# Kernel tuning notes

Measured on AMD Instinct MI355X. Metric: run time of the kernel, lower is better.

## Reference

```python
import jax, jax.numpy as jnp
import numpy as np

B, L, D, N = 8, 1024, 1024, 32  # N = d_state // 2 (complex conjugate-pair modes)
DT_MIN, DT_MAX = 0.001, 0.1


def setup_inputs() -> dict:
    key = jax.random.key(0)
    ks = jax.random.split(key, 12)
    s = 1.0 / np.sqrt(D)  # torch Linear / Conv1d default init bound
    inp = {
        "x": jax.random.normal(ks[0], (B, L, D), jnp.float32),
        "in_W": jax.random.uniform(ks[1], (D, D), jnp.float32, -s, s),
        "in_b": jax.random.uniform(ks[2], (D,), jnp.float32, -s, s),
        # S4D kernel params
        "log_dt": (np.log(DT_MIN)
                   + jax.random.uniform(ks[3], (D,), jnp.float32)
                   * (np.log(DT_MAX) - np.log(DT_MIN))).astype(jnp.float32),
        "C": jax.random.normal(ks[4], (D, N, 2), jnp.float32),  # complex C as (re, im)
        "log_A_real": jnp.log(0.5 * jnp.ones((D, N), jnp.float32)),
        "A_imag": jnp.tile((np.pi * jnp.arange(N, dtype=np.float32))[None, :], (D, 1)),
        "D_skip": jax.random.normal(ks[5], (D,), jnp.float32),
        # output_linear = Conv1d(D, 2D, 1) + GLU(dim=-2); kernel squeezed to (2D, D)
        "glu_W": jax.random.uniform(ks[6], (2 * D, D), jnp.float32, -s, s),
        "glu_b": jax.random.uniform(ks[7], (2 * D,), jnp.float32, -s, s),
        "out_W": jax.random.uniform(ks[8], (D, D), jnp.float32, -s, s),
        "out_b": jax.random.uniform(ks[9], (D,), jnp.float32, -s, s),
    }
    return inp


def reference(x, in_W, in_b, log_dt, C, log_A_real, A_imag, D_skip,
              glu_W, glu_b, out_W, out_b):
    # in_proj
    x_in = x @ in_W.T + in_b                      # (B, L, D)
    u = jnp.swapaxes(x_in, 1, 2)                  # (B, D, L) -- transposed=False path
    Lseq = u.shape[-1]

    # ---- S4D kernel (ZOH-like discretization of diagonal SSM) ----
    dt = jnp.exp(log_dt)                          # (D,)
    Cc = (C[..., 0] + 1j * C[..., 1]).astype(jnp.complex64)   # (D, N)
    A = (-jnp.exp(log_A_real) + 1j * A_imag).astype(jnp.complex64)
    dtA = A * dt[:, None].astype(jnp.complex64)   # (D, N)
    # Vandermonde: exp(dtA * l) for l in [0, L)
    K = jnp.exp(dtA[:, :, None] * jnp.arange(Lseq, dtype=jnp.float32))  # (D, N, L)
    Ceff = Cc * (jnp.exp(dtA) - 1.0) / A
    k = 2.0 * jnp.einsum('hn,hnl->hl', Ceff, K).real            # (D, L)

    # ---- FFT causal convolution ----
    n = 2 * Lseq
    k_f = jnp.fft.rfft(k, n=n)                    # (D, L+1)
    u_f = jnp.fft.rfft(u, n=n)                    # (B, D, L+1)
    y = jnp.fft.irfft(u_f * k_f, n=n)[..., :Lseq] # (B, D, L)

    y = y + u * D_skip[:, None]                   # skip connection
    y = jax.nn.gelu(y, approximate=False)         # torch nn.GELU (erf)

    # Conv1d(D, 2D, kernel=1) + GLU over channel dim
    z = jnp.einsum('oh,bhl->bol', glu_W, y) + glu_b[None, :, None]
    a, g = jnp.split(z, 2, axis=1)
    y = a * jax.nn.sigmoid(g)                     # (B, D, L)

    y = jnp.swapaxes(y, 1, 2)                     # (B, L, D)
    out = y @ out_W.T + out_b
    return out + x
```

## Files before the change

kernel.cpp:

```cpp
#include <hip/hip_runtime.h>
#include <math.h>

#define BB 8
#define LL 1024
#define DD 1024
#define KD 1024
#define NM 32
#define NCH 16
#define CL 64
#define NTOK (BB * LL)

typedef __bf16 bf16_t;
typedef __bf16 bf16x8 __attribute__((ext_vector_type(8)));
typedef __bf16 bf16x4 __attribute__((ext_vector_type(4)));
typedef float  f32x4  __attribute__((ext_vector_type(4)));

__device__ __forceinline__ float gelu_f(float z)
{
    float t = fmaf(0.044715f * z * z, z, z);
    return z / (1.f + expf(-1.5957691216f * t));
}

__global__ __launch_bounds__(256)
void f2b_all_kernel(const float* __restrict__ x,    bf16_t* __restrict__ xb,
                    const float* __restrict__ w0,   bf16_t* __restrict__ d0,
                    const float* __restrict__ w1,   bf16_t* __restrict__ d1,
                    const float* __restrict__ w2,   bf16_t* __restrict__ d2)
{
    int b = blockIdx.x;
    const float* s; bf16_t* d; int base;
    if (b < 8192)       { s = x;  d = xb; base = b; }
    else if (b < 9216)  { s = w0; d = d0; base = b - 8192; }
    else if (b < 11264) { s = w1; d = d1; base = b - 9216; }
    else                { s = w2; d = d2; base = b - 11264; }
    int i = (base * 256 + threadIdx.x) * 4;
    float4 f = *(const float4*)(s + i);
    bf16x4 o = { (bf16_t)f.x, (bf16_t)f.y, (bf16_t)f.z, (bf16_t)f.w };
    *(bf16x4*)(d + i) = o;
}

#define GLL(gp, lp) __builtin_amdgcn_global_load_lds( \
    (const __attribute__((address_space(1))) void*)(gp), \
    (__attribute__((address_space(3))) void*)(lp), 16, 0, 0)

__device__ __forceinline__ void stage_tile(const bf16_t* __restrict__ Ag,
                                           const bf16_t* __restrict__ Bg,
                                           bf16_t* Asb, bf16_t* Bsb, int tid)
{
    #pragma unroll
    for (int p = 0; p < 4; ++p) {
        int e = p * 256 + tid;
        int row = e >> 3, sc = ((e & 7) ^ (row & 7)) << 3;
        GLL(Ag + (size_t)row * KD + sc, Asb + e * 8);
    }
    #pragma unroll
    for (int p = 0; p < 4; ++p) {
        int e = p * 256 + tid;
        int row = e >> 3, sc = ((e & 7) ^ (row & 7)) << 3;
        GLL(Bg + (size_t)row * KD + sc, Bsb + e * 8);
    }
}

template<int MODE>
__global__ __launch_bounds__(256, 2)
void gemm_db_kernel(const bf16_t* __restrict__ A, const bf16_t* __restrict__ B,
                    const float* __restrict__ bias, const float* __restrict__ res,
                    void* __restrict__ outp, int ldo)
{
    __shared__ bf16_t As[2][128 * 64];
    __shared__ bf16_t Bs[2][128 * 64];
    const int tid = threadIdx.x;
    const int lane = tid & 63, w = tid >> 6;
    const int wy = w >> 1, wx = w & 1;
    const int m0 = blockIdx.y << 7, n0 = blockIdx.x << 7;
    const bf16_t* Ag = A + (size_t)m0 * KD;
    const bf16_t* Bg = B + (size_t)n0 * KD;
    f32x4 acc[4][4] = {};
    const int lm = lane & 15;
    const int qq = lane >> 4;

    stage_tile(Ag, Bg, As[0], Bs[0], tid);
    __syncthreads();

    int buf = 0;
    #pragma unroll 1
    for (int t = 0; t < 16; ++t) {
        if (t + 1 < 16)
            stage_tile(Ag + (t + 1) * 64, Bg + (t + 1) * 64,
                       As[buf ^ 1], Bs[buf ^ 1], tid);
        #pragma unroll
        for (int kk = 0; kk < 2; ++kk) {
            bf16x8 af[4], bfr[4];
            const int g = (kk << 2) + qq;
            #pragma unroll
            for (int i = 0; i < 4; ++i) {
                int row = (wy << 6) + (i << 4) + lm;
                af[i] = *(const bf16x8*)&As[buf][row * 64 + ((g ^ (row & 7)) << 3)];
            }
            #pragma unroll
            for (int j = 0; j < 4; ++j) {
                int row = (wx << 6) + (j << 4) + lm;
                bfr[j] = *(const bf16x8*)&Bs[buf][row * 64 + ((g ^ (row & 7)) << 3)];
            }
            #pragma unroll
            for (int i = 0; i < 4; ++i)
                #pragma unroll
                for (int j = 0; j < 4; ++j)
                    acc[i][j] = __builtin_amdgcn_mfma_f32_16x16x32_bf16(
                                    af[i], bfr[j], acc[i][j], 0, 0, 0);
        }
        __syncthreads();
        buf ^= 1;
    }

    const int row4 = (lane >> 4) << 2;
    #pragma unroll
    for (int i = 0; i < 4; ++i) {
        #pragma unroll
        for (int r = 0; r < 4; ++r) {
            int m = m0 + (wy << 6) + (i << 4) + row4 + r;
            #pragma unroll
            for (int j = 0; j < 4; ++j) {
                int n = n0 + (wx << 6) + (j << 4) + lm;
                float v = acc[i][j][r];
                if (MODE == 0) {
                    ((bf16_t*)outp)[(size_t)m * ldo + n] = (bf16_t)(v + bias[m]);
                } else if (MODE == 1) {
                    ((bf16_t*)outp)[(size_t)m * ldo + n] = (bf16_t)(v + bias[n]);
                } else {
                    ((float*)outp)[(size_t)m * ldo + n] =
                        v + bias[n] + res[(size_t)m * ldo + n];
                }
            }
        }
    }
}

__global__ __launch_bounds__(256)
void glu_combine_kernel(const bf16_t* __restrict__ z, bf16_t* __restrict__ v)
{
    int i = blockIdx.x * 256 + threadIdx.x;
    int m = i >> 7, n8 = (i & 127) << 3;
    const bf16_t* zp = z + (size_t)m * 2048 + n8;
    bf16x8 za = *(const bf16x8*)zp;
    bf16x8 zg = *(const bf16x8*)(zp + 1024);
    bf16x8 o;
    #pragma unroll
    for (int e = 0; e < 8; ++e) {
        float a = (float)za[e], gg = (float)zg[e];
        o[e] = (bf16_t)(a / (1.f + expf(-gg)));
    }
    *(bf16x8*)(v + (size_t)m * 1024 + n8) = o;
}

__global__ __launch_bounds__(64)
void genVTP_kernel(const float* __restrict__ log_dt, const float* __restrict__ lar,
                   const float* __restrict__ aim, const float* __restrict__ Cp,
                   const float* __restrict__ dskip,
                   bf16_t* __restrict__ V, bf16_t* __restrict__ TP)
{
    const int tid = threadIdx.x;
    if (blockIdx.x < DD / 2) {
        const int h = blockIdx.x * 2 + (tid >> 5);
        const int n = tid & 31;
        const float dt = expf(log_dt[h]);
        const float ardt = -expf(lar[h * NM + n]) * dt;
        const float aidt = aim[h * NM + n] * dt;
        float sn, cs;
        sincosf(aidt, &sn, &cs);
        float er = expf(ardt);
        float wr = er * cs, wi = er * sn;
        float inv = 1.f / fmaf(wr, wr, wi * wi);
        float vr = wr * inv, vi = -wi * inv;
        sincosf(63.f * aidt, &sn, &cs);
        er = expf(63.f * ardt);
        float pr = er * cs, pi = er * sn;
        bf16_t* rowr = V + ((size_t)h * 64 + 2 * n) * 64;
        bf16_t* rowi = rowr + 64;
        #pragma unroll
        for (int c8 = 0; c8 < 8; ++c8) {
            bf16x8 rr, ri;
            #pragma unroll
            for (int e = 0; e < 8; ++e) {
                rr[e] = (bf16_t)pr; ri[e] = (bf16_t)pi;
                float t = fmaf(pr, vr, -pi * vi);
                pi = fmaf(pr, vi, pi * vr);
                pr = t;
            }
            *(bf16x8*)(rowr + c8 * 8) = rr;
            *(bf16x8*)(rowi + c8 * 8) = ri;
        }
        return;
    }
    __shared__ float cr_s[NM], ci_s[NM], K_s[CL];
    __shared__ float wr_s[NM], wi_s[NM], ardt_s[NM], aidt_s[NM];
    __shared__ float er_s[65 * 33], ei_s[65 * 33];
    const int h = blockIdx.x - DD / 2;
    if (tid < NM) {
        int n = tid;
        const float dt = expf(log_dt[h]);
        float ar = -expf(lar[h * NM + n]);
        float ai = aim[h * NM + n];
        float sn, cs;
        sincosf(ai * dt, &sn, &cs);
        float er = expf(ar * dt);
        float wrr = er * cs, wii = er * sn;
        float Crr = Cp[(h * NM + n) * 2 + 0];
        float Cii = Cp[(h * NM + n) * 2 + 1];
        float nr = fmaf(Crr, wrr - 1.f, -Cii * wii);
        float ni = fmaf(Crr, wii, Cii * (wrr - 1.f));
        float inv = 2.f / fmaf(ar, ar, ai * ai);
        cr_s[n] = fmaf(nr, ar, ni * ai) * inv;
        ci_s[n] = fmaf(ni, ar, -nr * ai) * inv;
        wr_s[n] = wrr;  wi_s[n] = wii;
        ardt_s[n] = ar * dt;
        aidt_s[n] = ai * dt;
        er_s[n] = 1.f;  ei_s[n] = 0.f;
    }
    __syncthreads();
    {
        const int n = tid & 31;
        const int s = 1 + (tid >> 5) * 32;
        float sn, cs;
        sincosf(aidt_s[n] * (float)s, &sn, &cs);
        float e0 = expf(ardt_s[n] * (float)s);
        float pr = e0 * cs, pi = e0 * sn;
        const float wr = wr_s[n], wi = wi_s[n];
        int base = s * 33 + n;
        #pragma unroll
        for (int j = 0; j < 32; ++j) {
            er_s[base] = pr;  ei_s[base] = pi;
            float t0 = fmaf(pr, wr, -pi * wi);
            pi = fmaf(pr, wi, pi * wr);
            pr = t0;
            base += 33;
        }
    }
    __syncthreads();
    {
        const int d = tid;
        float kv = (d == 0) ? dskip[h] : 0.f;
        #pragma unroll
        for (int n = 0; n < NM; ++n) {
            kv = fmaf(cr_s[n], er_s[d * 33 + n], kv);
            kv = fmaf(-ci_s[n], ei_s[d * 33 + n], kv);
        }
        K_s[d] = kv;
    }
    __syncthreads();
    const int i = tid;
    bf16_t* row = TP + ((size_t)h * CL + i) * 128;
    #pragma unroll
    for (int c8 = 0; c8 < 8; ++c8) {
        bf16x8 v;
        #pragma unroll
        for (int e = 0; e < 8; ++e) {
            int l = c8 * 8 + e;
            v[e] = (l <= i) ? (bf16_t)K_s[i - l] : (bf16_t)0.f;
        }
        *(bf16x8*)(row + c8 * 8) = v;
    }
    #pragma unroll
    for (int c8 = 0; c8 < 8; ++c8) {
        bf16x8 v;
        #pragma unroll
        for (int q = 0; q < 4; ++q) {
            int n = c8 * 4 + q;
            float Wr = er_s[(i + 1) * 33 + n];
            float Wi = ei_s[(i + 1) * 33 + n];
            v[2 * q]     = (bf16_t)(fmaf(cr_s[n], Wr, -ci_s[n] * Wi));
            v[2 * q + 1] = (bf16_t)(-fmaf(cr_s[n], Wi, ci_s[n] * Wr));
        }
        *(bf16x8*)(row + 64 + c8 * 8) = v;
    }
}

__global__ __launch_bounds__(256)
void ssm_fused_kernel(const bf16_t* __restrict__ u_ch, const bf16_t* __restrict__ V,
                      const bf16_t* __restrict__ TP,
                      const float* __restrict__ log_dt, const float* __restrict__ lar,
                      const float* __restrict__ aim, bf16_t* __restrict__ y_bi)
{
    __shared__ float  Sbc_s[128 * 64];
    __shared__ bf16_t Sc_s[128 * 64];
    const int h = blockIdx.x;
    const int tid = threadIdx.x;
    const int lane = tid & 63, w = tid >> 6;
    const int lm = lane & 15, ks = (lane >> 4) << 3;
    const bf16_t* U   = u_ch + (size_t)h * 8192;
    const bf16_t* Vh  = V    + (size_t)h * 4096;
    const bf16_t* TPh = TP   + (size_t)h * 8192;

    bf16x8 af_u[2][2];
    #pragma unroll
    for (int im = 0; im < 2; ++im)
        #pragma unroll
        for (int kk = 0; kk < 2; ++kk)
            af_u[im][kk] = *(const bf16x8*)(U + (((w << 1) + im) * 16 + lm) * 64
                                            + kk * 32 + ks);

    f32x4 acc1[2][4] = {};
    #pragma unroll
    for (int kk = 0; kk < 2; ++kk) {
        bf16x8 bfr[4];
        #pragma unroll
        for (int jn = 0; jn < 4; ++jn)
            bfr[jn] = *(const bf16x8*)(Vh + (jn * 16 + lm) * 64 + kk * 32 + ks);
        #pragma unroll
        for (int im = 0; im < 2; ++im)
            #pragma unroll
            for (int jn = 0; jn < 4; ++jn)
                acc1[im][jn] = __builtin_amdgcn_mfma_f32_16x16x32_bf16(
                                   af_u[im][kk], bfr[jn], acc1[im][jn], 0, 0, 0);
    }
    const int r4 = (lane >> 4) << 2;
    #pragma unroll
    for (int im = 0; im < 2; ++im)
        #pragma unroll
        for (int jn = 0; jn < 4; ++jn)
            #pragma unroll
            for (int r = 0; r < 4; ++r)
                Sbc_s[(((w << 1) + im) * 16 + r4 + r) * 64 + jn * 16 + lm]
                    = acc1[im][jn][r];
    __syncthreads();

    {
        const int b = tid >> 5, n = tid & 31;
        const float dtv = expf(log_dt[h]);
        const float ardt = -expf(lar[h * NM + n]) * dtv;
        const float aidt = aim[h * NM + n] * dtv;
        float sn, cs;
        sincosf(64.f * aidt, &sn, &cs);
        float er = expf(64.f * ardt);
        const float gr = er * cs, gi = er * sn;
        float sr = 0.f, si = 0.f;
        for (int c = 0; c < NCH; ++c) {
            int idx = (b * 16 + c) * 64 + 2 * n;
            float lr = Sbc_s[idx], li = Sbc_s[idx + 1];
            Sc_s[idx]     = (bf16_t)sr;
            Sc_s[idx + 1] = (bf16_t)si;
            float t0 = fmaf(gr, sr, fmaf(-gi, si, lr));
            si = fmaf(gr, si, fmaf(gi, sr, li));
            sr = t0;
        }
    }
    __syncthreads();

    f32x4 acc2[2][4] = {};
    #pragma unroll
    for (int kk = 0; kk < 4; ++kk) {
        bf16x8 af[2], bfr[4];
        #pragma unroll
        for (int im = 0; im < 2; ++im) {
            if (kk < 2)
                af[im] = af_u[im][kk];
            else
                af[im] = *(bf16x8*)&Sc_s[(((w << 1) + im) * 16 + lm) * 64
                                         + (kk - 2) * 32 + ks];
        }
        #pragma unroll
        for (int jn = 0; jn < 4; ++jn)
            bfr[jn] = *(const bf16x8*)(TPh + (jn * 16 + lm) * 128 + kk * 32 + ks);
        #pragma unroll
        for (int im = 0; im < 2; ++im)
            #pragma unroll
            for (int jn = 0; jn < 4; ++jn)
                acc2[im][jn] = __builtin_amdgcn_mfma_f32_16x16x32_bf16(
                                   af[im], bfr[jn], acc2[im][jn], 0, 0, 0);
    }
    bf16_t* out = y_bi + (size_t)h * 8192;
    #pragma unroll
    for (int im = 0; im < 2; ++im)
        #pragma unroll
        for (int jn = 0; jn < 4; ++jn)
            #pragma unroll
            for (int r = 0; r < 4; ++r) {
                int batch = ((w << 1) + im) * 16 + r4 + r;
                int i = jn * 16 + lm;
                out[batch * 64 + i] = (bf16_t)gelu_f(acc2[im][jn][r]);
            }
}

__global__ __launch_bounds__(256)
void transpose_kernel(const bf16_t* __restrict__ src, bf16_t* __restrict__ dst,
                      int src_rows, int src_cols)
{
    __shared__ unsigned short tile[64][68];
    const int tid = threadIdx.x;
    const int c0 = blockIdx.x << 6, r0 = blockIdx.y << 6;
    const int r = tid >> 4, c4 = (tid & 15) << 2;
    #pragma unroll
    for (int p = 0; p < 4; ++p) {
        int rr = p * 16 + r;
        ushort4 v = *(const ushort4*)((const unsigned short*)src +
                                      (size_t)(r0 + rr) * src_cols + c0 + c4);
        *(ushort4*)&tile[rr][c4] = v;
    }
    __syncthreads();
    #pragma unroll
    for (int p = 0; p < 4; ++p) {
        int rr = p * 16 + r;
        ushort4 v;
        v.x = tile[c4 + 0][rr];
        v.y = tile[c4 + 1][rr];
        v.z = tile[c4 + 2][rr];
        v.w = tile[c4 + 3][rr];
        *(ushort4*)((unsigned short*)dst + (size_t)(c0 + rr) * src_rows + r0 + c4) = v;
    }
}

extern "C" void kernel_launch(void* const* d_in, const int* in_sizes, int n_in,
                              void* d_out, int out_size, void* d_ws, size_t ws_size,
                              hipStream_t stream)
{
    (void)in_sizes; (void)n_in; (void)out_size; (void)ws_size;
    const float* x      = (const float*)d_in[0];
    const float* in_W   = (const float*)d_in[1];
    const float* in_b   = (const float*)d_in[2];
    const float* log_dt = (const float*)d_in[3];
    const float* Cp     = (const float*)d_in[4];
    const float* lar    = (const float*)d_in[5];
    const float* aim    = (const float*)d_in[6];
    const float* dsk    = (const float*)d_in[7];
    const float* gluW   = (const float*)d_in[8];
    const float* glub   = (const float*)d_in[9];
    const float* outW   = (const float*)d_in[10];
    const float* outb   = (const float*)d_in[11];

    char* ws = (char*)d_ws;
    bf16_t* xb    = (bf16_t*)(ws);
    bf16_t* TP    = (bf16_t*)(ws);
    bf16_t* y_tok = (bf16_t*)(ws);
    bf16_t* vb    = (bf16_t*)(ws);
    bf16_t* V     = (bf16_t*)(ws + 16777216);
    bf16_t* z     = (bf16_t*)(ws + 16777216);
    bf16_t* u_ch  = (bf16_t*)(ws + 33554432);
    bf16_t* wbin  = (bf16_t*)(ws + 50331648);
    bf16_t* wbglu = (bf16_t*)(ws + 52428800);
    bf16_t* wbout = (bf16_t*)(ws + 56623104);
    bf16_t* y_bi  = (bf16_t*)d_out;

    f2b_all_kernel<<<dim3(12288), dim3(256), 0, stream>>>(
        x, xb, in_W, wbin, gluW, wbglu, outW, wbout);

    gemm_db_kernel<0><<<dim3(NTOK / 128, DD / 128), dim3(256), 0, stream>>>(
        wbin, xb, in_b, nullptr, u_ch, NTOK);

    genVTP_kernel<<<dim3(DD / 2 + DD), dim3(64), 0, stream>>>(
        log_dt, lar, aim, Cp, dsk, V, TP);
    ssm_fused_kernel<<<dim3(DD), dim3(256), 0, stream>>>(
        u_ch, V, TP, log_dt, lar, aim, y_bi);

    transpose_kernel<<<dim3(NTOK / 64, DD / 64), dim3(256), 0, stream>>>(y_bi, y_tok, DD, NTOK);
    gemm_db_kernel<1><<<dim3(2048 / 128, NTOK / 128), dim3(256), 0, stream>>>(
        y_tok, wbglu, glub, nullptr, z, 2048);
    glu_combine_kernel<<<dim3(NTOK * DD / 8 / 256), dim3(256), 0, stream>>>(z, vb);
    gemm_db_kernel<2><<<dim3(DD / 128, NTOK / 128), dim3(256), 0, stream>>>(
        vb, wbout, outb, x, d_out, DD);
}
```

Baseline: 258.4 us.

## Fuse GLU combine into GLU GEMM epilogue and remap block order

The GLU GEMM now computes both the value and gate halves for the same output tile in one block, running 32 K-steps into two accumulator sets and applying a*sigmoid(g) in the epilogue. This removes the separate glu_combine kernel and the round trip of the 2D-wide intermediate z through memory. Block IDs are also remapped across eight groups in all GEMM modes, aiming for better cache locality or XCD distribution. The cost is a second 64-register accumulator array, which raises register pressure and may reduce occupancy under the two-blocks-per-SM launch bound.

```diff
diff --git a/kernel.cpp b/kernel.cpp
--- a/kernel.cpp
+++ b/kernel.cpp
@@ -61,6 +61,34 @@
     }
 }
 
+__device__ __forceinline__ void tile_mfma(const bf16_t* __restrict__ Asb,
+                                          const bf16_t* __restrict__ Bsb,
+                                          int wy, int wx, int lm, int qq,
+                                          f32x4 (&ac)[4][4])
+{
+    #pragma unroll
+    for (int kk = 0; kk < 2; ++kk) {
+        bf16x8 af[4], bfr[4];
+        const int g = (kk << 2) + qq;
+        #pragma unroll
+        for (int i = 0; i < 4; ++i) {
+            int row = (wy << 6) + (i << 4) + lm;
+            af[i] = *(const bf16x8*)&Asb[row * 64 + ((g ^ (row & 7)) << 3)];
+        }
+        #pragma unroll
+        for (int j = 0; j < 4; ++j) {
+            int row = (wx << 6) + (j << 4) + lm;
+            bfr[j] = *(const bf16x8*)&Bsb[row * 64 + ((g ^ (row & 7)) << 3)];
+        }
+        #pragma unroll
+        for (int i = 0; i < 4; ++i)
+            #pragma unroll
+            for (int j = 0; j < 4; ++j)
+                ac[i][j] = __builtin_amdgcn_mfma_f32_16x16x32_bf16(
+                               af[i], bfr[j], ac[i][j], 0, 0, 0);
+    }
+}
+
 template<int MODE>
 __global__ __launch_bounds__(256, 2)
 void gemm_db_kernel(const bf16_t* __restrict__ A, const bf16_t* __restrict__ B,
@@ -72,43 +100,38 @@
     const int tid = threadIdx.x;
     const int lane = tid & 63, w = tid >> 6;
     const int wy = w >> 1, wx = w & 1;
-    const int m0 = blockIdx.y << 7, n0 = blockIdx.x << 7;
-    const bf16_t* Ag = A + (size_t)m0 * KD;
-    const bf16_t* Bg = B + (size_t)n0 * KD;
-    f32x4 acc[4][4] = {};
     const int lm = lane & 15;
     const int qq = lane >> 4;
 
-    stage_tile(Ag, Bg, As[0], Bs[0], tid);
+    const int nbx = gridDim.x;
+    int bid = blockIdx.y * nbx + blockIdx.x;
+    const int cpx = (gridDim.x * gridDim.y) >> 3;
+    bid = (bid & 7) * cpx + (bid >> 3);
+    const int m0 = (bid / nbx) << 7, n0 = (bid % nbx) << 7;
+
+    const bf16_t* Ag  = A + (size_t)m0 * KD;
+    const bf16_t* Bg0 = B + (size_t)n0 * KD;
+    const bf16_t* Bg1 = (MODE == 1) ? B + (size_t)(1024 + n0) * KD : Bg0;
+    const int NT = (MODE == 1) ? 32 : 16;
+
+    f32x4 acc[4][4]  = {};
+    f32x4 acc2[4][4] = {};
+
+    stage_tile(Ag, Bg0, As[0], Bs[0], tid);
     __syncthreads();
 
     int buf = 0;
     #pragma unroll 1
-    for (int t = 0; t < 16; ++t) {
-        if (t + 1 < 16)
-            stage_tile(Ag + (t + 1) * 64, Bg + (t + 1) * 64,
+    for (int t = 0; t < NT; ++t) {
+        if (t + 1 < NT) {
+            const bf16_t* Bn = (MODE == 1 && t + 1 >= 16) ? Bg1 : Bg0;
+            stage_tile(Ag + ((t + 1) & 15) * 64, Bn + ((t + 1) & 15) * 64,
                        As[buf ^ 1], Bs[buf ^ 1], tid);
-        #pragma unroll
-        for (int kk = 0; kk < 2; ++kk) {
-            bf16x8 af[4], bfr[4];
-            const int g = (kk << 2) + qq;
-            #pragma unroll
-            for (int i = 0; i < 4; ++i) {
-                int row = (wy << 6) + (i << 4) + lm;
-                af[i] = *(const bf16x8*)&As[buf][row * 64 + ((g ^ (row & 7)) << 3)];
-            }
-            #pragma unroll
-            for (int j = 0; j < 4; ++j) {
-                int row = (wx << 6) + (j << 4) + lm;
-                bfr[j] = *(const bf16x8*)&Bs[buf][row * 64 + ((g ^ (row & 7)) << 3)];
-            }
-            #pragma unroll
-            for (int i = 0; i < 4; ++i)
-                #pragma unroll
-                for (int j = 0; j < 4; ++j)
-                    acc[i][j] = __builtin_amdgcn_mfma_f32_16x16x32_bf16(
-                                    af[i], bfr[j], acc[i][j], 0, 0, 0);
-        }
+        }
+        if (MODE == 1 && t >= 16)
+            tile_mfma(As[buf], Bs[buf], wy, wx, lm, qq, acc2);
+        else
+            tile_mfma(As[buf], Bs[buf], wy, wx, lm, qq, acc);
         __syncthreads();
         buf ^= 1;
     }
@@ -126,7 +149,10 @@
                 if (MODE == 0) {
                     ((bf16_t*)outp)[(size_t)m * ldo + n] = (bf16_t)(v + bias[m]);
                 } else if (MODE == 1) {
-                    ((bf16_t*)outp)[(size_t)m * ldo + n] = (bf16_t)(v + bias[n]);
+                    float a = v + bias[n];
+                    float g = acc2[i][j][r] + bias[1024 + n];
+                    ((bf16_t*)outp)[(size_t)m * ldo + n] =
+                        (bf16_t)(a / (1.f + expf(-g)));
                 } else {
                     ((float*)outp)[(size_t)m * ldo + n] =
                         v + bias[n] + res[(size_t)m * ldo + n];
@@ -134,23 +160,6 @@
             }
         }
     }
-}
-
-__global__ __launch_bounds__(256)
-void glu_combine_kernel(const bf16_t* __restrict__ z, bf16_t* __restrict__ v)
-{
-    int i = blockIdx.x * 256 + threadIdx.x;
-    int m = i >> 7, n8 = (i & 127) << 3;
-    const bf16_t* zp = z + (size_t)m * 2048 + n8;
-    bf16x8 za = *(const bf16x8*)zp;
-    bf16x8 zg = *(const bf16x8*)(zp + 1024);
-    bf16x8 o;
-    #pragma unroll
-    for (int e = 0; e < 8; ++e) {
-        float a = (float)za[e], gg = (float)zg[e];
-        o[e] = (bf16_t)(a / (1.f + expf(-gg)));
-    }
-    *(bf16x8*)(v + (size_t)m * 1024 + n8) = o;
 }
 
 __global__ __launch_bounds__(64)
@@ -431,9 +440,8 @@
     bf16_t* xb    = (bf16_t*)(ws);
     bf16_t* TP    = (bf16_t*)(ws);
     bf16_t* y_tok = (bf16_t*)(ws);
-    bf16_t* vb    = (bf16_t*)(ws);
     bf16_t* V     = (bf16_t*)(ws + 16777216);
-    bf16_t* z     = (bf16_t*)(ws + 16777216);
+    bf16_t* vb    = (bf16_t*)(ws + 16777216);
     bf16_t* u_ch  = (bf16_t*)(ws + 33554432);
     bf16_t* wbin  = (bf16_t*)(ws + 50331648);
     bf16_t* wbglu = (bf16_t*)(ws + 52428800);
@@ -452,9 +460,9 @@
         u_ch, V, TP, log_dt, lar, aim, y_bi);
 
     transpose_kernel<<<dim3(NTOK / 64, DD / 64), dim3(256), 0, stream>>>(y_bi, y_tok, DD, NTOK);
-    gemm_db_kernel<1><<<dim3(2048 / 128, NTOK / 128), dim3(256), 0, stream>>>(
-        y_tok, wbglu, glub, nullptr, z, 2048);
-    glu_combine_kernel<<<dim3(NTOK * DD / 8 / 256), dim3(256), 0, stream>>>(z, vb);
+    gemm_db_kernel<1><<<dim3(1024 / 128, NTOK / 128), dim3(256), 0, stream>>>(
+        y_tok, wbglu, glub, nullptr, vb, 1024);
+
     gemm_db_kernel<2><<<dim3(DD / 128, NTOK / 128), dim3(256), 0, stream>>>(
         vb, wbout, outb, x, d_out, DD);
 }
```

New measurement: 258.6 us. No clear change (+0.1%).
